# Kernel optimization log

Hardware: AMD Instinct MI355X
Metric: run time of the kernel (lower is better)

The kernel has to match this reference:

```python
import jax, jax.numpy as jnp
import numpy as np

N_NODES = 100000
N_EDGES = 1600000
NODE_DIM = 64
HIDDEN = 64
T = 11


def _init_linear(key, d_in, d_out, bias=True):
    kw, kb = jax.random.split(key)
    lim = 1.0 / np.sqrt(d_in)
    W = jax.random.uniform(kw, (d_in, d_out), jnp.float32, -lim, lim)
    if bias:
        b = jax.random.uniform(kb, (d_out,), jnp.float32, -lim, lim)
        return W, b
    return W


def setup_inputs() -> dict:
    key = jax.random.key(0)
    ks = jax.random.split(key, 10)
    x = jax.random.normal(ks[0], (N_NODES, NODE_DIM), jnp.float32)
    edge_index = jax.random.randint(ks[1], (2, N_EDGES), 0, N_NODES, jnp.int64)
    time_span = jnp.arange(T, dtype=jnp.float32)
    # SAGEConv params: W_neigh (lin_l, with bias) applied to mean-aggregated
    # neighbors, W_root (lin_r, no bias) applied to the node itself.
    W1n, b1 = _init_linear(ks[2], NODE_DIM, HIDDEN)
    W1r = _init_linear(ks[3], NODE_DIM, HIDDEN, bias=False)
    W2n, b2 = _init_linear(ks[4], HIDDEN, HIDDEN)
    W2r = _init_linear(ks[5], HIDDEN, HIDDEN, bias=False)
    W3n, b3 = _init_linear(ks[6], HIDDEN, NODE_DIM)
    W3r = _init_linear(ks[7], HIDDEN, NODE_DIM, bias=False)
    Wd, bd = _init_linear(ks[8], NODE_DIM, 2)
    return {
        "x": x, "edge_index": edge_index, "time_span": time_span,
        "W1n": W1n, "b1": b1, "W1r": W1r,
        "W2n": W2n, "b2": b2, "W2r": W2r,
        "W3n": W3n, "b3": b3, "W3r": W3r,
        "Wd": Wd, "bd": bd,
    }


def _sage_conv(x, src, dst, deg_inv, Wn, bn, Wr):
    # gather source features, mean-aggregate onto targets (PyG SAGEConv 'mean')
    agg = jax.ops.segment_sum(x[src], dst, num_segments=N_NODES)  # [N, d]
    mean = agg * deg_inv  # zero for isolated nodes
    return mean @ Wn + bn + x @ Wr


def reference(x, edge_index, time_span, W1n, b1, W1r, W2n, b2, W2r,
              W3n, b3, W3r, Wd, bd):
    src, dst = edge_index[0], edge_index[1]
    deg = jax.ops.segment_sum(jnp.ones((N_EDGES,), jnp.float32), dst,
                              num_segments=N_NODES)
    deg_inv = jnp.where(deg > 0, 1.0 / jnp.maximum(deg, 1.0), 0.0)[:, None]

    def ode_func(h):
        h1 = jax.nn.relu(_sage_conv(h, src, dst, deg_inv, W1n, b1, W1r))
        h2 = jax.nn.relu(_sage_conv(h1, src, dst, deg_inv, W2n, b2, W2r))
        return _sage_conv(h2, src, dst, deg_inv, W3n, b3, W3r)

    dts = time_span[1:] - time_span[:-1]  # euler fixed-step per interval

    def step(h, dt):
        h_new = h + dt * ode_func(h)
        return h_new, h_new

    _, xs = jax.lax.scan(step, x, dts)
    solution = jnp.concatenate([x[None], xs], axis=0)  # [T, N, node_dim]
    trajectories = solution @ Wd + bd  # [T, N, 2]
    return trajectories, solution
```

## Files before the change

kernel.cpp:

```cpp
#include <hip/hip_runtime.h>

#define NN 100000
#define NE 1600000
#define DIM 64
#define TT 11
#define NB_SCAN 391

typedef unsigned short u16;
typedef unsigned int u32;

__device__ __forceinline__ u32 pack_bf16(float a, float b) {
    u32 ua = __float_as_uint(a);
    ua += 0x7fff + ((ua >> 16) & 1);
    u32 ub = __float_as_uint(b);
    ub += 0x7fff + ((ub >> 16) & 1);
    return (ua >> 16) | (ub & 0xffff0000u);
}

__global__ void k_deg(const int* __restrict__ dst, int* __restrict__ deg) {
    int e = blockIdx.x * blockDim.x + threadIdx.x;
    if (e < NE) atomicAdd(&deg[dst[e]], 1);
}

__global__ __launch_bounds__(256) void k_bsum(const int* __restrict__ deg,
                                              int* __restrict__ bsum) {
    __shared__ int s[256];
    int t = threadIdx.x;
    int i = blockIdx.x * 256 + t;
    s[t] = (i < NN) ? deg[i] : 0;
    __syncthreads();
    for (int off = 128; off >= 1; off >>= 1) {
        if (t < off) s[t] += s[t + off];
        __syncthreads();
    }
    if (t == 0) bsum[blockIdx.x] = s[0];
}

__global__ __launch_bounds__(512) void k_scan1(const int* __restrict__ bsum,
                                               int* __restrict__ bpre) {
    __shared__ int s[512];
    int t = threadIdx.x;
    int v0 = (t < NB_SCAN) ? bsum[t] : 0;
    s[t] = v0;
    __syncthreads();
    for (int off = 1; off < 512; off <<= 1) {
        int v = (t >= off) ? s[t - off] : 0;
        __syncthreads();
        s[t] += v;
        __syncthreads();
    }
    if (t < NB_SCAN) bpre[t] = s[t] - v0;
}

__global__ __launch_bounds__(256) void k_rowptr(const int* __restrict__ deg,
        const int* __restrict__ bpre, int* __restrict__ row_ptr,
        int* __restrict__ cursor, float* __restrict__ deg_inv) {
    __shared__ int s[256];
    int t = threadIdx.x;
    int i = blockIdx.x * 256 + t;
    int d = (i < NN) ? deg[i] : 0;
    s[t] = d;
    __syncthreads();
    for (int off = 1; off < 256; off <<= 1) {
        int v = (t >= off) ? s[t - off] : 0;
        __syncthreads();
        s[t] += v;
        __syncthreads();
    }
    if (i < NN) {
        int excl = bpre[blockIdx.x] + s[t] - d;
        row_ptr[i] = excl;
        cursor[i] = excl;
        deg_inv[i] = d > 0 ? 1.0f / (float)d : 0.0f;
        if (i == NN - 1) row_ptr[NN] = excl + d;
    }
}

__global__ void k_fill(const int* __restrict__ src, const int* __restrict__ dst,
        int* __restrict__ cursor, int* __restrict__ csr_src) {
    int e = blockIdx.x * blockDim.x + threadIdx.x;
    if (e < NE) {
        int p = atomicAdd(&cursor[dst[e]], 1);
        csr_src[p] = src[e];
    }
}

__global__ __launch_bounds__(256) void k_gather(const u16* __restrict__ hb,
        const int* __restrict__ row_ptr, const int* __restrict__ csr_src,
        const float* __restrict__ deg_inv, float* __restrict__ M) {
    int wid = (int)((blockIdx.x * blockDim.x + threadIdx.x) >> 6);
    int lane = threadIdx.x & 63;
    if (wid >= NN) return;
    int sub = lane >> 3;
    int d4 = lane & 7;
    int b = row_ptr[wid], e = row_ptr[wid + 1];
    float di = deg_inv[wid];
    float a0[8] = {0, 0, 0, 0, 0, 0, 0, 0};
    float a1[8] = {0, 0, 0, 0, 0, 0, 0, 0};
    int i = b;
    for (; i + 16 <= e; i += 16) {
        int n0 = csr_src[i + sub];
        int n1 = csr_src[i + 8 + sub];
        uint4 v0 = *(const uint4*)(hb + ((size_t)n0 << 6) + d4 * 8);
        uint4 v1 = *(const uint4*)(hb + ((size_t)n1 << 6) + d4 * 8);
        const u32* w0 = (const u32*)&v0;
        const u32* w1 = (const u32*)&v1;
#pragma unroll
        for (int w = 0; w < 4; ++w) {
            a0[2 * w]     += __uint_as_float(w0[w] << 16);
            a0[2 * w + 1] += __uint_as_float(w0[w] & 0xffff0000u);
            a1[2 * w]     += __uint_as_float(w1[w] << 16);
            a1[2 * w + 1] += __uint_as_float(w1[w] & 0xffff0000u);
        }
    }
    if (i + 8 <= e) {
        int n0 = csr_src[i + sub];
        uint4 v0 = *(const uint4*)(hb + ((size_t)n0 << 6) + d4 * 8);
        const u32* w0 = (const u32*)&v0;
#pragma unroll
        for (int w = 0; w < 4; ++w) {
            a0[2 * w]     += __uint_as_float(w0[w] << 16);
            a0[2 * w + 1] += __uint_as_float(w0[w] & 0xffff0000u);
        }
        i += 8;
    }
    if (sub < e - i) {
        int n1 = csr_src[i + sub];
        uint4 v1 = *(const uint4*)(hb + ((size_t)n1 << 6) + d4 * 8);
        const u32* w1 = (const u32*)&v1;
#pragma unroll
        for (int w = 0; w < 4; ++w) {
            a1[2 * w]     += __uint_as_float(w1[w] << 16);
            a1[2 * w + 1] += __uint_as_float(w1[w] & 0xffff0000u);
        }
    }
    float s[8];
#pragma unroll
    for (int k = 0; k < 8; ++k) {
        float v = a0[k] + a1[k];
        v += __shfl_xor(v, 32);
        v += __shfl_xor(v, 16);
        v += __shfl_xor(v, 8);
        s[k] = v * di;
    }
    if (lane < 8) {
        float4* mr = (float4*)(M + ((size_t)wid << 6)) + d4 * 2;
        mr[0] = make_float4(s[0], s[1], s[2], s[3]);
        mr[1] = make_float4(s[4], s[5], s[6], s[7]);
    }
}

template <int MODE>
__global__ __launch_bounds__(256) void k_transform(
        const float* __restrict__ M, const float* __restrict__ H,
        const float* __restrict__ Wn, const float* __restrict__ bias,
        const float* __restrict__ Wr, const float* __restrict__ prev,
        const float* __restrict__ ts, int tstep, float* __restrict__ out,
        u16* __restrict__ out_b,
        const float* __restrict__ Wd, const float* __restrict__ bd,
        float* __restrict__ traj) {
    __shared__ float Ws[128 * 64];
    __shared__ float tp0[MODE ? 128 * 9 : 1];
    __shared__ float tp1[MODE ? 128 * 9 : 1];
    int tid = threadIdx.x;
    {
        const float4* wn4 = (const float4*)Wn;
        const float4* wr4 = (const float4*)Wr;
        float4* ws4 = (float4*)Ws;
        for (int i = tid; i < 2048; i += 256)
            ws4[i] = (i < 1024) ? wn4[i] : wr4[i - 1024];
    }
    __syncthreads();
    int jg = tid & 7, ng = tid >> 3;
    int nbase = blockIdx.x * 128 + ng * 4;
    int j0 = jg * 8;
    float acc[4][8];
#pragma unroll
    for (int i = 0; i < 4; ++i)
#pragma unroll
        for (int j = 0; j < 8; ++j) acc[i][j] = bias[j0 + j];
    int nidx[4];
    bool valid[4];
#pragma unroll
    for (int i = 0; i < 4; ++i) {
        int n = nbase + i;
        valid[i] = n < NN;
        nidx[i] = valid[i] ? n : 0;
    }
#pragma unroll 1
    for (int ph = 0; ph < 2; ++ph) {
        const float* A = ph ? H : M;
        int wofs = ph ? 64 * 64 : 0;
        for (int k0 = 0; k0 < 64; k0 += 4) {
            float a[4][4];
#pragma unroll
            for (int i = 0; i < 4; ++i)
                *(float4*)a[i] = *(const float4*)(A + (size_t)nidx[i] * 64 + k0);
#pragma unroll
            for (int kk = 0; kk < 4; ++kk) {
                float w[8];
                *(float4*)&w[0] = *(float4*)&Ws[wofs + (k0 + kk) * 64 + j0];
                *(float4*)&w[4] = *(float4*)&Ws[wofs + (k0 + kk) * 64 + j0 + 4];
#pragma unroll
                for (int i = 0; i < 4; ++i)
#pragma unroll
                    for (int j = 0; j < 8; ++j)
                        acc[i][j] = fmaf(a[i][kk], w[j], acc[i][j]);
            }
        }
    }
    float dt = 0.f, wd0[8], wd1[8];
    if (MODE == 1) {
        dt = ts[tstep + 1] - ts[tstep];
#pragma unroll
        for (int j = 0; j < 8; ++j) {
            wd0[j] = Wd[(j0 + j) * 2 + 0];
            wd1[j] = Wd[(j0 + j) * 2 + 1];
        }
    }
#pragma unroll
    for (int i = 0; i < 4; ++i) {
        float o[8];
        float p0 = 0.f, p1 = 0.f;
#pragma unroll
        for (int j = 0; j < 8; ++j) {
            float v = acc[i][j];
            if (MODE == 0) v = fmaxf(v, 0.f);
            else v = prev[(size_t)nidx[i] * 64 + j0 + j] + dt * v;
            o[j] = v;
            if (MODE == 1) { p0 = fmaf(v, wd0[j], p0); p1 = fmaf(v, wd1[j], p1); }
        }
        if (MODE == 1) {
            tp0[(ng * 4 + i) * 9 + jg] = p0;
            tp1[(ng * 4 + i) * 9 + jg] = p1;
        }
        if (valid[i]) {
            *(float4*)(out + (size_t)nidx[i] * 64 + j0) = *(float4*)&o[0];
            *(float4*)(out + (size_t)nidx[i] * 64 + j0 + 4) = *(float4*)&o[4];
            uint4 pb;
            pb.x = pack_bf16(o[0], o[1]);
            pb.y = pack_bf16(o[2], o[3]);
            pb.z = pack_bf16(o[4], o[5]);
            pb.w = pack_bf16(o[6], o[7]);
            *(uint4*)(out_b + (size_t)nidx[i] * 64 + j0) = pb;
        }
    }
    if (MODE == 1) {
        __syncthreads();
        int node = tid >> 1, comp = tid & 1;
        const float* tp = comp ? tp1 : tp0;
        float s = bd[comp];
#pragma unroll
        for (int g = 0; g < 8; ++g) s += tp[node * 9 + g];
        int gnode = blockIdx.x * 128 + node;
        if (gnode < NN)
            traj[((size_t)(tstep + 1) * NN + gnode) * 2 + comp] = s;
    }
}

__global__ __launch_bounds__(256) void k_init(const float* __restrict__ x,
        const float* __restrict__ Wd, const float* __restrict__ bd,
        float* __restrict__ sol0, u16* __restrict__ xb,
        float* __restrict__ traj) {
    int n = blockIdx.x * blockDim.x + threadIdx.x;
    if (n >= NN) return;
    const float4* xr = (const float4*)(x + ((size_t)n << 6));
    float4* sr = (float4*)(sol0 + ((size_t)n << 6));
    uint4* br = (uint4*)(xb + ((size_t)n << 6));
    float p0 = bd[0], p1 = bd[1];
#pragma unroll
    for (int k8 = 0; k8 < 8; ++k8) {
        float4 v0 = xr[k8 * 2];
        float4 v1 = xr[k8 * 2 + 1];
        sr[k8 * 2] = v0;
        sr[k8 * 2 + 1] = v1;
        uint4 pb;
        pb.x = pack_bf16(v0.x, v0.y);
        pb.y = pack_bf16(v0.z, v0.w);
        pb.z = pack_bf16(v1.x, v1.y);
        pb.w = pack_bf16(v1.z, v1.w);
        br[k8] = pb;
        int k = k8 * 8;
        p0 = fmaf(v0.x, Wd[(k + 0) * 2], p0); p1 = fmaf(v0.x, Wd[(k + 0) * 2 + 1], p1);
        p0 = fmaf(v0.y, Wd[(k + 1) * 2], p0); p1 = fmaf(v0.y, Wd[(k + 1) * 2 + 1], p1);
        p0 = fmaf(v0.z, Wd[(k + 2) * 2], p0); p1 = fmaf(v0.z, Wd[(k + 2) * 2 + 1], p1);
        p0 = fmaf(v0.w, Wd[(k + 3) * 2], p0); p1 = fmaf(v0.w, Wd[(k + 3) * 2 + 1], p1);
        p0 = fmaf(v1.x, Wd[(k + 4) * 2], p0); p1 = fmaf(v1.x, Wd[(k + 4) * 2 + 1], p1);
        p0 = fmaf(v1.y, Wd[(k + 5) * 2], p0); p1 = fmaf(v1.y, Wd[(k + 5) * 2 + 1], p1);
        p0 = fmaf(v1.z, Wd[(k + 6) * 2], p0); p1 = fmaf(v1.z, Wd[(k + 6) * 2 + 1], p1);
        p0 = fmaf(v1.w, Wd[(k + 7) * 2], p0); p1 = fmaf(v1.w, Wd[(k + 7) * 2 + 1], p1);
    }
    traj[(size_t)n * 2 + 0] = p0;
    traj[(size_t)n * 2 + 1] = p1;
}

extern "C" void kernel_launch(void* const* d_in, const int* in_sizes, int n_in,
                              void* d_out, int out_size, void* d_ws, size_t ws_size,
                              hipStream_t stream) {
    const float* x = (const float*)d_in[0];
    const int* ei = (const int*)d_in[1];
    const float* ts = (const float*)d_in[2];
    const float* W1n = (const float*)d_in[3];
    const float* b1 = (const float*)d_in[4];
    const float* W1r = (const float*)d_in[5];
    const float* W2n = (const float*)d_in[6];
    const float* b2 = (const float*)d_in[7];
    const float* W2r = (const float*)d_in[8];
    const float* W3n = (const float*)d_in[9];
    const float* b3 = (const float*)d_in[10];
    const float* W3r = (const float*)d_in[11];
    const float* Wd = (const float*)d_in[12];
    const float* bd = (const float*)d_in[13];
    const int* src = ei;
    const int* dst = ei + NE;

    char* w = (char*)d_ws;
    int* deg = (int*)w;          w += (size_t)NN * 4;
    int* row_ptr = (int*)w;      w += (size_t)(NN + 1) * 4;
    int* cursor = (int*)w;       w += (size_t)NN * 4;
    float* deg_inv = (float*)w;  w += (size_t)NN * 4;
    int* bsum = (int*)w;         w += (size_t)512 * 4;
    int* bpre = (int*)w;         w += (size_t)512 * 4;
    int* csr = (int*)w;          w += (size_t)NE * 4;
    float* M = (float*)w;        w += (size_t)NN * DIM * 4;
    float* h1 = (float*)w;       w += (size_t)NN * DIM * 4;
    float* h2 = (float*)w;       w += (size_t)NN * DIM * 4;
    u16* hb0 = (u16*)w;          w += (size_t)NN * DIM * 2;
    u16* hb1 = (u16*)w;          w += (size_t)NN * DIM * 2;
    u16* hb2 = (u16*)w;          w += (size_t)NN * DIM * 2;

    float* traj = (float*)d_out;
    float* sol = traj + (size_t)TT * NN * 2;

    hipMemsetAsync(deg, 0, (size_t)NN * 4, stream);
    k_deg<<<(NE + 255) / 256, 256, 0, stream>>>(dst, deg);
    k_bsum<<<NB_SCAN, 256, 0, stream>>>(deg, bsum);
    k_scan1<<<1, 512, 0, stream>>>(bsum, bpre);
    k_rowptr<<<NB_SCAN, 256, 0, stream>>>(deg, bpre, row_ptr, cursor, deg_inv);
    k_fill<<<(NE + 255) / 256, 256, 0, stream>>>(src, dst, cursor, csr);
    k_init<<<NB_SCAN, 256, 0, stream>>>(x, Wd, bd, sol, hb0, traj);

    const int GB = (NN * 64 + 255) / 256;
    const int TB = (NN + 127) / 128;
    for (int t = 0; t < TT - 1; ++t) {
        float* st = sol + (size_t)t * NN * DIM;
        float* sn = st + (size_t)NN * DIM;
        k_gather<<<GB, 256, 0, stream>>>(hb0, row_ptr, csr, deg_inv, M);
        k_transform<0><<<TB, 256, 0, stream>>>(M, st, W1n, b1, W1r, nullptr, ts, t, h1, hb1, Wd, bd, traj);
        k_gather<<<GB, 256, 0, stream>>>(hb1, row_ptr, csr, deg_inv, M);
        k_transform<0><<<TB, 256, 0, stream>>>(M, h1, W2n, b2, W2r, nullptr, ts, t, h2, hb2, Wd, bd, traj);
        k_gather<<<GB, 256, 0, stream>>>(hb2, row_ptr, csr, deg_inv, M);
        k_transform<1><<<TB, 256, 0, stream>>>(M, h2, W3n, b3, W3r, st, ts, t, sn, hb0, Wd, bd, traj);
    }
}
```

Before: 2.811 ms.

## Fuse neighbor gather into transform kernel via shared-memory bf16 aggregate tile

Merges the separate gather and transform kernels into one k_conv kernel: each block first aggregates neighbor means for its 128 nodes into a bf16 shared-memory tile, then runs the dense transform from shared memory. This removes the global M buffer round-trip (write then read of NN×64 floats) and halves kernel launches. The cost is lower gather parallelism (one block of 4 waves walks 128 nodes serially, 782 blocks total) and an extra bf16 rounding of the mean aggregate. The trajectory scratch is aliased onto the weight tile after a sync, and occupancy is pinned with a launch bound of 3 blocks per SIMD.

```diff
diff --git a/kernel.cpp b/kernel.cpp
--- a/kernel.cpp
+++ b/kernel.cpp
@@ -15,6 +15,9 @@
     u32 ub = __float_as_uint(b);
     ub += 0x7fff + ((ub >> 16) & 1);
     return (ua >> 16) | (ub & 0xffff0000u);
+}
+__device__ __forceinline__ float bf2f(u16 v) {
+    return __uint_as_float(((u32)v) << 16);
 }
 
 __global__ void k_deg(const int* __restrict__ dst, int* __restrict__ deg) {
@@ -85,83 +88,20 @@
     }
 }
 
-__global__ __launch_bounds__(256) void k_gather(const u16* __restrict__ hb,
+#define MS_LD 68
+template <int MODE>
+__global__ __launch_bounds__(256, 3) void k_conv(
+        const u16* __restrict__ hb, const float* __restrict__ H,
         const int* __restrict__ row_ptr, const int* __restrict__ csr_src,
-        const float* __restrict__ deg_inv, float* __restrict__ M) {
-    int wid = (int)((blockIdx.x * blockDim.x + threadIdx.x) >> 6);
-    int lane = threadIdx.x & 63;
-    if (wid >= NN) return;
-    int sub = lane >> 3;
-    int d4 = lane & 7;
-    int b = row_ptr[wid], e = row_ptr[wid + 1];
-    float di = deg_inv[wid];
-    float a0[8] = {0, 0, 0, 0, 0, 0, 0, 0};
-    float a1[8] = {0, 0, 0, 0, 0, 0, 0, 0};
-    int i = b;
-    for (; i + 16 <= e; i += 16) {
-        int n0 = csr_src[i + sub];
-        int n1 = csr_src[i + 8 + sub];
-        uint4 v0 = *(const uint4*)(hb + ((size_t)n0 << 6) + d4 * 8);
-        uint4 v1 = *(const uint4*)(hb + ((size_t)n1 << 6) + d4 * 8);
-        const u32* w0 = (const u32*)&v0;
-        const u32* w1 = (const u32*)&v1;
-#pragma unroll
-        for (int w = 0; w < 4; ++w) {
-            a0[2 * w]     += __uint_as_float(w0[w] << 16);
-            a0[2 * w + 1] += __uint_as_float(w0[w] & 0xffff0000u);
-            a1[2 * w]     += __uint_as_float(w1[w] << 16);
-            a1[2 * w + 1] += __uint_as_float(w1[w] & 0xffff0000u);
-        }
-    }
-    if (i + 8 <= e) {
-        int n0 = csr_src[i + sub];
-        uint4 v0 = *(const uint4*)(hb + ((size_t)n0 << 6) + d4 * 8);
-        const u32* w0 = (const u32*)&v0;
-#pragma unroll
-        for (int w = 0; w < 4; ++w) {
-            a0[2 * w]     += __uint_as_float(w0[w] << 16);
-            a0[2 * w + 1] += __uint_as_float(w0[w] & 0xffff0000u);
-        }
-        i += 8;
-    }
-    if (sub < e - i) {
-        int n1 = csr_src[i + sub];
-        uint4 v1 = *(const uint4*)(hb + ((size_t)n1 << 6) + d4 * 8);
-        const u32* w1 = (const u32*)&v1;
-#pragma unroll
-        for (int w = 0; w < 4; ++w) {
-            a1[2 * w]     += __uint_as_float(w1[w] << 16);
-            a1[2 * w + 1] += __uint_as_float(w1[w] & 0xffff0000u);
-        }
-    }
-    float s[8];
-#pragma unroll
-    for (int k = 0; k < 8; ++k) {
-        float v = a0[k] + a1[k];
-        v += __shfl_xor(v, 32);
-        v += __shfl_xor(v, 16);
-        v += __shfl_xor(v, 8);
-        s[k] = v * di;
-    }
-    if (lane < 8) {
-        float4* mr = (float4*)(M + ((size_t)wid << 6)) + d4 * 2;
-        mr[0] = make_float4(s[0], s[1], s[2], s[3]);
-        mr[1] = make_float4(s[4], s[5], s[6], s[7]);
-    }
-}
-
-template <int MODE>
-__global__ __launch_bounds__(256) void k_transform(
-        const float* __restrict__ M, const float* __restrict__ H,
+        const float* __restrict__ deg_inv,
         const float* __restrict__ Wn, const float* __restrict__ bias,
         const float* __restrict__ Wr, const float* __restrict__ prev,
-        const float* __restrict__ ts, int tstep, float* __restrict__ out,
-        u16* __restrict__ out_b,
+        const float* __restrict__ ts, int tstep,
+        float* __restrict__ out, u16* __restrict__ out_b,
         const float* __restrict__ Wd, const float* __restrict__ bd,
         float* __restrict__ traj) {
     __shared__ float Ws[128 * 64];
-    __shared__ float tp0[MODE ? 128 * 9 : 1];
-    __shared__ float tp1[MODE ? 128 * 9 : 1];
+    __shared__ u16 Ms[128 * MS_LD];
     int tid = threadIdx.x;
     {
         const float4* wn4 = (const float4*)Wn;
@@ -170,9 +110,77 @@
         for (int i = tid; i < 2048; i += 256)
             ws4[i] = (i < 1024) ? wn4[i] : wr4[i - 1024];
     }
+    int wv = tid >> 6, lane = tid & 63;
+    int sub = lane >> 3, d4 = lane & 7;
+    for (int ni = 0; ni < 32; ++ni) {
+        int lrow = wv * 32 + ni;
+        int node = blockIdx.x * 128 + lrow;
+        if (node >= NN) break;
+        int b = row_ptr[node], e = row_ptr[node + 1];
+        float di = deg_inv[node];
+        float a0[8] = {0, 0, 0, 0, 0, 0, 0, 0};
+        float a1[8] = {0, 0, 0, 0, 0, 0, 0, 0};
+        int i = b;
+        for (; i + 16 <= e; i += 16) {
+            int n0 = csr_src[i + sub];
+            int n1 = csr_src[i + 8 + sub];
+            uint4 v0 = *(const uint4*)(hb + ((size_t)n0 << 6) + d4 * 8);
+            uint4 v1 = *(const uint4*)(hb + ((size_t)n1 << 6) + d4 * 8);
+            const u32* w0 = (const u32*)&v0;
+            const u32* w1 = (const u32*)&v1;
+#pragma unroll
+            for (int w = 0; w < 4; ++w) {
+                a0[2 * w]     += __uint_as_float(w0[w] << 16);
+                a0[2 * w + 1] += __uint_as_float(w0[w] & 0xffff0000u);
+                a1[2 * w]     += __uint_as_float(w1[w] << 16);
+                a1[2 * w + 1] += __uint_as_float(w1[w] & 0xffff0000u);
+            }
+        }
+        if (i + 8 <= e) {
+            int n0 = csr_src[i + sub];
+            uint4 v0 = *(const uint4*)(hb + ((size_t)n0 << 6) + d4 * 8);
+            const u32* w0 = (const u32*)&v0;
+#pragma unroll
+            for (int w = 0; w < 4; ++w) {
+                a0[2 * w]     += __uint_as_float(w0[w] << 16);
+                a0[2 * w + 1] += __uint_as_float(w0[w] & 0xffff0000u);
+            }
+            i += 8;
+        }
+        if (sub < e - i) {
+            int n1 = csr_src[i + sub];
+            uint4 v1 = *(const uint4*)(hb + ((size_t)n1 << 6) + d4 * 8);
+            const u32* w1 = (const u32*)&v1;
+#pragma unroll
+            for (int w = 0; w < 4; ++w) {
+                a1[2 * w]     += __uint_as_float(w1[w] << 16);
+                a1[2 * w + 1] += __uint_as_float(w1[w] & 0xffff0000u);
+            }
+        }
+        float s[8];
+#pragma unroll
+        for (int k = 0; k < 8; ++k) {
+            float v = a0[k] + a1[k];
+            v += __shfl_xor(v, 32);
+            v += __shfl_xor(v, 16);
+            v += __shfl_xor(v, 8);
+            s[k] = v * di;
+        }
+        if (lane < 8) {
+            uint2 pa, pb;
+            pa.x = pack_bf16(s[0], s[1]);
+            pa.y = pack_bf16(s[2], s[3]);
+            pb.x = pack_bf16(s[4], s[5]);
+            pb.y = pack_bf16(s[6], s[7]);
+            u16* mp = &Ms[lrow * MS_LD + d4 * 8];
+            *(uint2*)mp = pa;
+            *(uint2*)(mp + 4) = pb;
+        }
+    }
     __syncthreads();
     int jg = tid & 7, ng = tid >> 3;
     int nbase = blockIdx.x * 128 + ng * 4;
+    int lbase = ng * 4;
     int j0 = jg * 8;
     float acc[4][8];
 #pragma unroll
@@ -187,26 +195,41 @@
         valid[i] = n < NN;
         nidx[i] = valid[i] ? n : 0;
     }
-#pragma unroll 1
-    for (int ph = 0; ph < 2; ++ph) {
-        const float* A = ph ? H : M;
-        int wofs = ph ? 64 * 64 : 0;
-        for (int k0 = 0; k0 < 64; k0 += 4) {
-            float a[4][4];
+    for (int k0 = 0; k0 < 64; k0 += 4) {
+        float a[4][4];
+#pragma unroll
+        for (int i = 0; i < 4; ++i) {
+            ushort4 r = *(const ushort4*)&Ms[(lbase + i) * MS_LD + k0];
+            a[i][0] = bf2f(r.x); a[i][1] = bf2f(r.y);
+            a[i][2] = bf2f(r.z); a[i][3] = bf2f(r.w);
+        }
+#pragma unroll
+        for (int kk = 0; kk < 4; ++kk) {
+            float w[8];
+            *(float4*)&w[0] = *(float4*)&Ws[(k0 + kk) * 64 + j0];
+            *(float4*)&w[4] = *(float4*)&Ws[(k0 + kk) * 64 + j0 + 4];
 #pragma unroll
             for (int i = 0; i < 4; ++i)
-                *(float4*)a[i] = *(const float4*)(A + (size_t)nidx[i] * 64 + k0);
-#pragma unroll
-            for (int kk = 0; kk < 4; ++kk) {
-                float w[8];
-                *(float4*)&w[0] = *(float4*)&Ws[wofs + (k0 + kk) * 64 + j0];
-                *(float4*)&w[4] = *(float4*)&Ws[wofs + (k0 + kk) * 64 + j0 + 4];
-#pragma unroll
-                for (int i = 0; i < 4; ++i)
-#pragma unroll
-                    for (int j = 0; j < 8; ++j)
-                        acc[i][j] = fmaf(a[i][kk], w[j], acc[i][j]);
-            }
+#pragma unroll
+                for (int j = 0; j < 8; ++j)
+                    acc[i][j] = fmaf(a[i][kk], w[j], acc[i][j]);
+        }
+    }
+    for (int k0 = 0; k0 < 64; k0 += 4) {
+        float a[4][4];
+#pragma unroll
+        for (int i = 0; i < 4; ++i)
+            *(float4*)a[i] = *(const float4*)(H + (size_t)nidx[i] * 64 + k0);
+#pragma unroll
+        for (int kk = 0; kk < 4; ++kk) {
+            float w[8];
+            *(float4*)&w[0] = *(float4*)&Ws[4096 + (k0 + kk) * 64 + j0];
+            *(float4*)&w[4] = *(float4*)&Ws[4096 + (k0 + kk) * 64 + j0 + 4];
+#pragma unroll
+            for (int i = 0; i < 4; ++i)
+#pragma unroll
+                for (int j = 0; j < 8; ++j)
+                    acc[i][j] = fmaf(a[i][kk], w[j], acc[i][j]);
         }
     }
     float dt = 0.f, wd0[8], wd1[8];
@@ -217,7 +240,10 @@
             wd0[j] = Wd[(j0 + j) * 2 + 0];
             wd1[j] = Wd[(j0 + j) * 2 + 1];
         }
-    }
+        __syncthreads();
+    }
+    float* tp0 = Ws;
+    float* tp1 = Ws + 128 * 9;
 #pragma unroll
     for (int i = 0; i < 4; ++i) {
         float o[8];
@@ -322,7 +348,6 @@
     int* bsum = (int*)w;         w += (size_t)512 * 4;
     int* bpre = (int*)w;         w += (size_t)512 * 4;
     int* csr = (int*)w;          w += (size_t)NE * 4;
-    float* M = (float*)w;        w += (size_t)NN * DIM * 4;
     float* h1 = (float*)w;       w += (size_t)NN * DIM * 4;
     float* h2 = (float*)w;       w += (size_t)NN * DIM * 4;
     u16* hb0 = (u16*)w;          w += (size_t)NN * DIM * 2;
@@ -340,16 +365,15 @@
     k_fill<<<(NE + 255) / 256, 256, 0, stream>>>(src, dst, cursor, csr);
     k_init<<<NB_SCAN, 256, 0, stream>>>(x, Wd, bd, sol, hb0, traj);
 
-    const int GB = (NN * 64 + 255) / 256;
     const int TB = (NN + 127) / 128;
     for (int t = 0; t < TT - 1; ++t) {
         float* st = sol + (size_t)t * NN * DIM;
         float* sn = st + (size_t)NN * DIM;
-        k_gather<<<GB, 256, 0, stream>>>(hb0, row_ptr, csr, deg_inv, M);
-        k_transform<0><<<TB, 256, 0, stream>>>(M, st, W1n, b1, W1r, nullptr, ts, t, h1, hb1, Wd, bd, traj);
-        k_gather<<<GB, 256, 0, stream>>>(hb1, row_ptr, csr, deg_inv, M);
-        k_transform<0><<<TB, 256, 0, stream>>>(M, h1, W2n, b2, W2r, nullptr, ts, t, h2, hb2, Wd, bd, traj);
-        k_gather<<<GB, 256, 0, stream>>>(hb2, row_ptr, csr, deg_inv, M);
-        k_transform<1><<<TB, 256, 0, stream>>>(M, h2, W3n, b3, W3r, st, ts, t, sn, hb0, Wd, bd, traj);
-    }
-}
+        k_conv<0><<<TB, 256, 0, stream>>>(hb0, st, row_ptr, csr, deg_inv,
+                W1n, b1, W1r, nullptr, ts, t, h1, hb1, Wd, bd, traj);
+        k_conv<0><<<TB, 256, 0, stream>>>(hb1, h1, row_ptr, csr, deg_inv,
+                W2n, b2, W2r, nullptr, ts, t, h2, hb2, Wd, bd, traj);
+        k_conv<1><<<TB, 256, 0, stream>>>(hb2, h2, row_ptr, csr, deg_inv,
+                W3n, b3, W3r, st, ts, t, sn, hb0, Wd, bd, traj);
+    }
+}
```

After: 4.693 ms. +66.9%, slower.

## Use bf16 activations in transform and bucket CSR neighbors by source chunk

Applied to the files above, without the earlier changes.

Stores the mean-aggregated features in bf16 and has the transform kernels read bf16 copies of both aggregated and root features. This halves their read traffic and drops the fp32 h1/h2 intermediate writes. The CSR build now orders each node's neighbor list by source-index chunk, so gathers touch nearby rows together and cache locality should improve. In exchange, the root term loses precision through bf16 rounding, and the setup needs a larger per-node chunk count array plus an extra memset and atomics.

```diff
diff --git a/kernel.cpp b/kernel.cpp
--- a/kernel.cpp
+++ b/kernel.cpp
@@ -5,6 +5,8 @@
 #define DIM 64
 #define TT 11
 #define NB_SCAN 391
+#define NCH 13
+#define CST 16
 
 typedef unsigned short u16;
 typedef unsigned int u32;
@@ -16,10 +18,18 @@
     ub += 0x7fff + ((ub >> 16) & 1);
     return (ua >> 16) | (ub & 0xffff0000u);
 }
-
-__global__ void k_deg(const int* __restrict__ dst, int* __restrict__ deg) {
+__device__ __forceinline__ float bf2f(u16 v) {
+    return __uint_as_float(((u32)v) << 16);
+}
+
+__global__ void k_degc(const int* __restrict__ src, const int* __restrict__ dst,
+                       int* __restrict__ deg, int* __restrict__ degc) {
     int e = blockIdx.x * blockDim.x + threadIdx.x;
-    if (e < NE) atomicAdd(&deg[dst[e]], 1);
+    if (e < NE) {
+        int d = dst[e], c = src[e] >> 13;
+        atomicAdd(&deg[d], 1);
+        atomicAdd(&degc[d * CST + c], 1);
+    }
 }
 
 __global__ __launch_bounds__(256) void k_bsum(const int* __restrict__ deg,
@@ -53,8 +63,9 @@
 }
 
 __global__ __launch_bounds__(256) void k_rowptr(const int* __restrict__ deg,
-        const int* __restrict__ bpre, int* __restrict__ row_ptr,
-        int* __restrict__ cursor, float* __restrict__ deg_inv) {
+        const int* __restrict__ degc, const int* __restrict__ bpre,
+        int* __restrict__ row_ptr, int* __restrict__ cursor16,
+        float* __restrict__ deg_inv) {
     __shared__ int s[256];
     int t = threadIdx.x;
     int i = blockIdx.x * 256 + t;
@@ -70,24 +81,30 @@
     if (i < NN) {
         int excl = bpre[blockIdx.x] + s[t] - d;
         row_ptr[i] = excl;
-        cursor[i] = excl;
         deg_inv[i] = d > 0 ? 1.0f / (float)d : 0.0f;
+        int run = excl;
+#pragma unroll
+        for (int c = 0; c < NCH; ++c) {
+            cursor16[i * CST + c] = run;
+            run += degc[i * CST + c];
+        }
         if (i == NN - 1) row_ptr[NN] = excl + d;
     }
 }
 
-__global__ void k_fill(const int* __restrict__ src, const int* __restrict__ dst,
-        int* __restrict__ cursor, int* __restrict__ csr_src) {
+__global__ void k_fillc(const int* __restrict__ src, const int* __restrict__ dst,
+        int* __restrict__ cursor16, int* __restrict__ csr_src) {
     int e = blockIdx.x * blockDim.x + threadIdx.x;
     if (e < NE) {
-        int p = atomicAdd(&cursor[dst[e]], 1);
-        csr_src[p] = src[e];
+        int sv = src[e];
+        int p = atomicAdd(&cursor16[dst[e] * CST + (sv >> 13)], 1);
+        csr_src[p] = sv;
     }
 }
 
 __global__ __launch_bounds__(256) void k_gather(const u16* __restrict__ hb,
         const int* __restrict__ row_ptr, const int* __restrict__ csr_src,
-        const float* __restrict__ deg_inv, float* __restrict__ M) {
+        const float* __restrict__ deg_inv, u16* __restrict__ Mb) {
     int wid = (int)((blockIdx.x * blockDim.x + threadIdx.x) >> 6);
     int lane = threadIdx.x & 63;
     if (wid >= NN) return;
@@ -144,15 +161,18 @@
         s[k] = v * di;
     }
     if (lane < 8) {
-        float4* mr = (float4*)(M + ((size_t)wid << 6)) + d4 * 2;
-        mr[0] = make_float4(s[0], s[1], s[2], s[3]);
-        mr[1] = make_float4(s[4], s[5], s[6], s[7]);
+        uint4 p;
+        p.x = pack_bf16(s[0], s[1]);
+        p.y = pack_bf16(s[2], s[3]);
+        p.z = pack_bf16(s[4], s[5]);
+        p.w = pack_bf16(s[6], s[7]);
+        *(uint4*)(Mb + ((size_t)wid << 6) + d4 * 8) = p;
     }
 }
 
 template <int MODE>
 __global__ __launch_bounds__(256) void k_transform(
-        const float* __restrict__ M, const float* __restrict__ H,
+        const u16* __restrict__ Mb, const u16* __restrict__ Hb,
         const float* __restrict__ Wn, const float* __restrict__ bias,
         const float* __restrict__ Wr, const float* __restrict__ prev,
         const float* __restrict__ ts, int tstep, float* __restrict__ out,
@@ -189,13 +209,16 @@
     }
 #pragma unroll 1
     for (int ph = 0; ph < 2; ++ph) {
-        const float* A = ph ? H : M;
+        const u16* A = ph ? Hb : Mb;
         int wofs = ph ? 64 * 64 : 0;
         for (int k0 = 0; k0 < 64; k0 += 4) {
             float a[4][4];
 #pragma unroll
-            for (int i = 0; i < 4; ++i)
-                *(float4*)a[i] = *(const float4*)(A + (size_t)nidx[i] * 64 + k0);
+            for (int i = 0; i < 4; ++i) {
+                ushort4 r = *(const ushort4*)(A + ((size_t)nidx[i] << 6) + k0);
+                a[i][0] = bf2f(r.x); a[i][1] = bf2f(r.y);
+                a[i][2] = bf2f(r.z); a[i][3] = bf2f(r.w);
+            }
 #pragma unroll
             for (int kk = 0; kk < 4; ++kk) {
                 float w[8];
@@ -235,8 +258,10 @@
             tp1[(ng * 4 + i) * 9 + jg] = p1;
         }
         if (valid[i]) {
-            *(float4*)(out + (size_t)nidx[i] * 64 + j0) = *(float4*)&o[0];
-            *(float4*)(out + (size_t)nidx[i] * 64 + j0 + 4) = *(float4*)&o[4];
+            if (MODE == 1) {
+                *(float4*)(out + (size_t)nidx[i] * 64 + j0) = *(float4*)&o[0];
+                *(float4*)(out + (size_t)nidx[i] * 64 + j0 + 4) = *(float4*)&o[4];
+            }
             uint4 pb;
             pb.x = pack_bf16(o[0], o[1]);
             pb.y = pack_bf16(o[2], o[3]);
@@ -316,15 +341,14 @@
 
     char* w = (char*)d_ws;
     int* deg = (int*)w;          w += (size_t)NN * 4;
+    int* degc = (int*)w;         w += (size_t)NN * CST * 4;
     int* row_ptr = (int*)w;      w += (size_t)(NN + 1) * 4;
-    int* cursor = (int*)w;       w += (size_t)NN * 4;
+    int* cursor16 = (int*)w;     w += (size_t)NN * CST * 4;
     float* deg_inv = (float*)w;  w += (size_t)NN * 4;
     int* bsum = (int*)w;         w += (size_t)512 * 4;
     int* bpre = (int*)w;         w += (size_t)512 * 4;
     int* csr = (int*)w;          w += (size_t)NE * 4;
-    float* M = (float*)w;        w += (size_t)NN * DIM * 4;
-    float* h1 = (float*)w;       w += (size_t)NN * DIM * 4;
-    float* h2 = (float*)w;       w += (size_t)NN * DIM * 4;
+    u16* Mb = (u16*)w;           w += (size_t)NN * DIM * 2;
     u16* hb0 = (u16*)w;          w += (size_t)NN * DIM * 2;
     u16* hb1 = (u16*)w;          w += (size_t)NN * DIM * 2;
     u16* hb2 = (u16*)w;          w += (size_t)NN * DIM * 2;
@@ -332,12 +356,12 @@
     float* traj = (float*)d_out;
     float* sol = traj + (size_t)TT * NN * 2;
 
-    hipMemsetAsync(deg, 0, (size_t)NN * 4, stream);
-    k_deg<<<(NE + 255) / 256, 256, 0, stream>>>(dst, deg);
+    hipMemsetAsync(deg, 0, (size_t)NN * (CST + 1) * 4, stream);
+    k_degc<<<(NE + 255) / 256, 256, 0, stream>>>(src, dst, deg, degc);
     k_bsum<<<NB_SCAN, 256, 0, stream>>>(deg, bsum);
     k_scan1<<<1, 512, 0, stream>>>(bsum, bpre);
-    k_rowptr<<<NB_SCAN, 256, 0, stream>>>(deg, bpre, row_ptr, cursor, deg_inv);
-    k_fill<<<(NE + 255) / 256, 256, 0, stream>>>(src, dst, cursor, csr);
+    k_rowptr<<<NB_SCAN, 256, 0, stream>>>(deg, degc, bpre, row_ptr, cursor16, deg_inv);
+    k_fillc<<<(NE + 255) / 256, 256, 0, stream>>>(src, dst, cursor16, csr);
     k_init<<<NB_SCAN, 256, 0, stream>>>(x, Wd, bd, sol, hb0, traj);
 
     const int GB = (NN * 64 + 255) / 256;
@@ -345,11 +369,14 @@
     for (int t = 0; t < TT - 1; ++t) {
         float* st = sol + (size_t)t * NN * DIM;
         float* sn = st + (size_t)NN * DIM;
-        k_gather<<<GB, 256, 0, stream>>>(hb0, row_ptr, csr, deg_inv, M);
-        k_transform<0><<<TB, 256, 0, stream>>>(M, st, W1n, b1, W1r, nullptr, ts, t, h1, hb1, Wd, bd, traj);
-        k_gather<<<GB, 256, 0, stream>>>(hb1, row_ptr, csr, deg_inv, M);
-        k_transform<0><<<TB, 256, 0, stream>>>(M, h1, W2n, b2, W2r, nullptr, ts, t, h2, hb2, Wd, bd, traj);
-        k_gather<<<GB, 256, 0, stream>>>(hb2, row_ptr, csr, deg_inv, M);
-        k_transform<1><<<TB, 256, 0, stream>>>(M, h2, W3n, b3, W3r, st, ts, t, sn, hb0, Wd, bd, traj);
-    }
-}
+        k_gather<<<GB, 256, 0, stream>>>(hb0, row_ptr, csr, deg_inv, Mb);
+        k_transform<0><<<TB, 256, 0, stream>>>(Mb, hb0, W1n, b1, W1r, nullptr,
+                ts, t, nullptr, hb1, Wd, bd, traj);
+        k_gather<<<GB, 256, 0, stream>>>(hb1, row_ptr, csr, deg_inv, Mb);
+        k_transform<0><<<TB, 256, 0, stream>>>(Mb, hb1, W2n, b2, W2r, nullptr,
+                ts, t, nullptr, hb2, Wd, bd, traj);
+        k_gather<<<GB, 256, 0, stream>>>(hb2, row_ptr, csr, deg_inv, Mb);
+        k_transform<1><<<TB, 256, 0, stream>>>(Mb, hb2, W3n, b3, W3r, st,
+                ts, t, sn, hb0, Wd, bd, traj);
+    }
+}
```

Result: faster. 2.725 ms (-3.1%).

## Use bf16 MFMA for SAGE transforms and keep intermediates in bf16

Applied to the files above, without the earlier changes.

Replaces the fp32 FMA-based dense transform with bf16 MFMA 16x16x32 instructions, using weights pre-transposed and packed to bf16 by a new prep kernel. The gather now writes the mean aggregate as bf16, and the transform reads bf16 node features directly, so the fp32 M, h1 and h2 buffers and their writes are dropped. The epilogue is staged through LDS so each thread handles half a node row, and the trajectory projection uses a shuffle reduction. The intent is to cut memory traffic and ALU time in the transform. The trade-off is bf16 rounding of the root-term inputs and of the aggregates, which lowers precision.

```diff
diff --git a/kernel.cpp b/kernel.cpp
--- a/kernel.cpp
+++ b/kernel.cpp
@@ -8,6 +8,8 @@
 
 typedef unsigned short u16;
 typedef unsigned int u32;
+typedef __attribute__((ext_vector_type(8))) short bf16x8;
+typedef __attribute__((ext_vector_type(4))) float f32x4;
 
 __device__ __forceinline__ u32 pack_bf16(float a, float b) {
     u32 ua = __float_as_uint(a);
@@ -85,9 +87,27 @@
     }
 }
 
+__global__ __launch_bounds__(256) void k_wprep(
+        const float* __restrict__ W1n, const float* __restrict__ W1r,
+        const float* __restrict__ W2n, const float* __restrict__ W2r,
+        const float* __restrict__ W3n, const float* __restrict__ W3r,
+        u16* __restrict__ Wt) {
+    const float* Ws[6] = {W1n, W1r, W2n, W2r, W3n, W3r};
+    const float* W = Ws[blockIdx.x];
+    u16* o = Wt + blockIdx.x * 4096;
+    int t = threadIdx.x;
+    int n = t >> 2, kg = (t & 3) * 16;
+    u32 pk[8];
+#pragma unroll
+    for (int j = 0; j < 8; ++j)
+        pk[j] = pack_bf16(W[(kg + 2 * j) * 64 + n], W[(kg + 2 * j + 1) * 64 + n]);
+    *(uint4*)(o + n * 64 + kg)     = make_uint4(pk[0], pk[1], pk[2], pk[3]);
+    *(uint4*)(o + n * 64 + kg + 8) = make_uint4(pk[4], pk[5], pk[6], pk[7]);
+}
+
 __global__ __launch_bounds__(256) void k_gather(const u16* __restrict__ hb,
         const int* __restrict__ row_ptr, const int* __restrict__ csr_src,
-        const float* __restrict__ deg_inv, float* __restrict__ M) {
+        const float* __restrict__ deg_inv, u16* __restrict__ Mb) {
     int wid = (int)((blockIdx.x * blockDim.x + threadIdx.x) >> 6);
     int lane = threadIdx.x & 63;
     if (wid >= NN) return;
@@ -144,117 +164,157 @@
         s[k] = v * di;
     }
     if (lane < 8) {
-        float4* mr = (float4*)(M + ((size_t)wid << 6)) + d4 * 2;
-        mr[0] = make_float4(s[0], s[1], s[2], s[3]);
-        mr[1] = make_float4(s[4], s[5], s[6], s[7]);
+        uint4 p;
+        p.x = pack_bf16(s[0], s[1]);
+        p.y = pack_bf16(s[2], s[3]);
+        p.z = pack_bf16(s[4], s[5]);
+        p.w = pack_bf16(s[6], s[7]);
+        *(uint4*)(Mb + ((size_t)wid << 6) + d4 * 8) = p;
     }
 }
 
 template <int MODE>
 __global__ __launch_bounds__(256) void k_transform(
-        const float* __restrict__ M, const float* __restrict__ H,
-        const float* __restrict__ Wn, const float* __restrict__ bias,
-        const float* __restrict__ Wr, const float* __restrict__ prev,
+        const u16* __restrict__ Mb, const u16* __restrict__ Hb,
+        const u16* __restrict__ Wtn, const float* __restrict__ bias,
+        const u16* __restrict__ Wtr, const float* __restrict__ prev,
         const float* __restrict__ ts, int tstep, float* __restrict__ out,
         u16* __restrict__ out_b,
         const float* __restrict__ Wd, const float* __restrict__ bd,
         float* __restrict__ traj) {
-    __shared__ float Ws[128 * 64];
-    __shared__ float tp0[MODE ? 128 * 9 : 1];
-    __shared__ float tp1[MODE ? 128 * 9 : 1];
+    __shared__ float Ls[4][32 * 68];
+    __shared__ float WdS[128];
     int tid = threadIdx.x;
+    if (MODE == 1 && tid < 128) WdS[tid] = Wd[tid];
+    int wv = tid >> 6, lane = tid & 63;
+    int r16 = lane & 15, kq = lane >> 4;
+    int nodeW = blockIdx.x * 128 + wv * 32;
+    size_t rowA[2];
+#pragma unroll
+    for (int rt = 0; rt < 2; ++rt) {
+        int n = nodeW + rt * 16 + r16;
+        rowA[rt] = (size_t)(n < NN ? n : NN - 1) << 6;
+    }
+    f32x4 acc[2][4];
+#pragma unroll
+    for (int ct = 0; ct < 4; ++ct) {
+        float bc = bias[ct * 16 + r16];
+#pragma unroll
+        for (int rt = 0; rt < 2; ++rt)
+            acc[rt][ct] = (f32x4){bc, bc, bc, bc};
+    }
     {
-        const float4* wn4 = (const float4*)Wn;
-        const float4* wr4 = (const float4*)Wr;
-        float4* ws4 = (float4*)Ws;
-        for (int i = tid; i < 2048; i += 256)
-            ws4[i] = (i < 1024) ? wn4[i] : wr4[i - 1024];
-    }
+        bf16x8 a[2][2], b[4][2];
+#pragma unroll
+        for (int rt = 0; rt < 2; ++rt)
+#pragma unroll
+            for (int kh = 0; kh < 2; ++kh)
+                a[rt][kh] = *(const bf16x8*)(Mb + rowA[rt] + kh * 32 + kq * 8);
+#pragma unroll
+        for (int ct = 0; ct < 4; ++ct)
+#pragma unroll
+            for (int kh = 0; kh < 2; ++kh)
+                b[ct][kh] = *(const bf16x8*)(Wtn + (ct * 16 + r16) * 64 + kh * 32 + kq * 8);
+#pragma unroll
+        for (int rt = 0; rt < 2; ++rt)
+#pragma unroll
+            for (int ct = 0; ct < 4; ++ct)
+#pragma unroll
+                for (int kh = 0; kh < 2; ++kh)
+                    acc[rt][ct] = __builtin_amdgcn_mfma_f32_16x16x32_bf16(
+                        a[rt][kh], b[ct][kh], acc[rt][ct], 0, 0, 0);
+    }
+    {
+        bf16x8 a[2][2], b[4][2];
+#pragma unroll
+        for (int rt = 0; rt < 2; ++rt)
+#pragma unroll
+            for (int kh = 0; kh < 2; ++kh)
+                a[rt][kh] = *(const bf16x8*)(Hb + rowA[rt] + kh * 32 + kq * 8);
+#pragma unroll
+        for (int ct = 0; ct < 4; ++ct)
+#pragma unroll
+            for (int kh = 0; kh < 2; ++kh)
+                b[ct][kh] = *(const bf16x8*)(Wtr + (ct * 16 + r16) * 64 + kh * 32 + kq * 8);
+#pragma unroll
+        for (int rt = 0; rt < 2; ++rt)
+#pragma unroll
+            for (int ct = 0; ct < 4; ++ct)
+#pragma unroll
+                for (int kh = 0; kh < 2; ++kh)
+                    acc[rt][ct] = __builtin_amdgcn_mfma_f32_16x16x32_bf16(
+                        a[rt][kh], b[ct][kh], acc[rt][ct], 0, 0, 0);
+    }
+    float* L = Ls[wv];
+#pragma unroll
+    for (int rt = 0; rt < 2; ++rt)
+#pragma unroll
+        for (int ct = 0; ct < 4; ++ct)
+#pragma unroll
+            for (int j = 0; j < 4; ++j)
+                L[(rt * 16 + kq * 4 + j) * 68 + ct * 16 + r16] = acc[rt][ct][j];
     __syncthreads();
-    int jg = tid & 7, ng = tid >> 3;
-    int nbase = blockIdx.x * 128 + ng * 4;
-    int j0 = jg * 8;
-    float acc[4][8];
-#pragma unroll
-    for (int i = 0; i < 4; ++i)
-#pragma unroll
-        for (int j = 0; j < 8; ++j) acc[i][j] = bias[j0 + j];
-    int nidx[4];
-    bool valid[4];
-#pragma unroll
-    for (int i = 0; i < 4; ++i) {
-        int n = nbase + i;
-        valid[i] = n < NN;
-        nidx[i] = valid[i] ? n : 0;
-    }
-#pragma unroll 1
-    for (int ph = 0; ph < 2; ++ph) {
-        const float* A = ph ? H : M;
-        int wofs = ph ? 64 * 64 : 0;
-        for (int k0 = 0; k0 < 64; k0 += 4) {
-            float a[4][4];
-#pragma unroll
-            for (int i = 0; i < 4; ++i)
-                *(float4*)a[i] = *(const float4*)(A + (size_t)nidx[i] * 64 + k0);
-#pragma unroll
-            for (int kk = 0; kk < 4; ++kk) {
-                float w[8];
-                *(float4*)&w[0] = *(float4*)&Ws[wofs + (k0 + kk) * 64 + j0];
-                *(float4*)&w[4] = *(float4*)&Ws[wofs + (k0 + kk) * 64 + j0 + 4];
-#pragma unroll
-                for (int i = 0; i < 4; ++i)
-#pragma unroll
-                    for (int j = 0; j < 8; ++j)
-                        acc[i][j] = fmaf(a[i][kk], w[j], acc[i][j]);
-            }
-        }
-    }
-    float dt = 0.f, wd0[8], wd1[8];
+    int nl = tid >> 1, hf = tid & 1;
+    int gnode = blockIdx.x * 128 + nl;
+    const float* Lrow = &Ls[nl >> 5][(nl & 31) * 68 + hf * 32];
+    float dt = 0.f;
+    if (MODE == 1) dt = ts[tstep + 1] - ts[tstep];
+    float v[32];
+    float p0 = 0.f, p1 = 0.f;
+    bool ok = gnode < NN;
+    size_t gofs = ((size_t)(ok ? gnode : 0) << 6) + hf * 32;
+#pragma unroll
+    for (int i = 0; i < 32; ++i) {
+        float x = Lrow[i];
+        if (MODE == 0) x = fmaxf(x, 0.f);
+        v[i] = x;
+    }
     if (MODE == 1) {
-        dt = ts[tstep + 1] - ts[tstep];
-#pragma unroll
-        for (int j = 0; j < 8; ++j) {
-            wd0[j] = Wd[(j0 + j) * 2 + 0];
-            wd1[j] = Wd[(j0 + j) * 2 + 1];
-        }
-    }
-#pragma unroll
-    for (int i = 0; i < 4; ++i) {
-        float o[8];
-        float p0 = 0.f, p1 = 0.f;
-#pragma unroll
-        for (int j = 0; j < 8; ++j) {
-            float v = acc[i][j];
-            if (MODE == 0) v = fmaxf(v, 0.f);
-            else v = prev[(size_t)nidx[i] * 64 + j0 + j] + dt * v;
-            o[j] = v;
-            if (MODE == 1) { p0 = fmaf(v, wd0[j], p0); p1 = fmaf(v, wd1[j], p1); }
-        }
+#pragma unroll
+        for (int i4 = 0; i4 < 8; ++i4) {
+            float4 pv = *(const float4*)(prev + gofs + i4 * 4);
+            v[i4 * 4 + 0] = pv.x + dt * v[i4 * 4 + 0];
+            v[i4 * 4 + 1] = pv.y + dt * v[i4 * 4 + 1];
+            v[i4 * 4 + 2] = pv.z + dt * v[i4 * 4 + 2];
+            v[i4 * 4 + 3] = pv.w + dt * v[i4 * 4 + 3];
+        }
+#pragma unroll
+        for (int i = 0; i < 32; ++i) {
+            p0 = fmaf(v[i], WdS[(hf * 32 + i) * 2 + 0], p0);
+            p1 = fmaf(v[i], WdS[(hf * 32 + i) * 2 + 1], p1);
+        }
+    }
+    if (ok) {
         if (MODE == 1) {
-            tp0[(ng * 4 + i) * 9 + jg] = p0;
-            tp1[(ng * 4 + i) * 9 + jg] = p1;
-        }
-        if (valid[i]) {
-            *(float4*)(out + (size_t)nidx[i] * 64 + j0) = *(float4*)&o[0];
-            *(float4*)(out + (size_t)nidx[i] * 64 + j0 + 4) = *(float4*)&o[4];
+#pragma unroll
+            for (int i4 = 0; i4 < 8; ++i4)
+                *(float4*)(out + gofs + i4 * 4) =
+                    make_float4(v[i4 * 4], v[i4 * 4 + 1], v[i4 * 4 + 2], v[i4 * 4 + 3]);
+        }
+#pragma unroll
+        for (int q = 0; q < 2; ++q) {
             uint4 pb;
-            pb.x = pack_bf16(o[0], o[1]);
-            pb.y = pack_bf16(o[2], o[3]);
-            pb.z = pack_bf16(o[4], o[5]);
-            pb.w = pack_bf16(o[6], o[7]);
-            *(uint4*)(out_b + (size_t)nidx[i] * 64 + j0) = pb;
+            pb.x = pack_bf16(v[q * 16 + 0], v[q * 16 + 1]);
+            pb.y = pack_bf16(v[q * 16 + 2], v[q * 16 + 3]);
+            pb.z = pack_bf16(v[q * 16 + 4], v[q * 16 + 5]);
+            pb.w = pack_bf16(v[q * 16 + 6], v[q * 16 + 7]);
+            uint4 pc;
+            pc.x = pack_bf16(v[q * 16 + 8], v[q * 16 + 9]);
+            pc.y = pack_bf16(v[q * 16 + 10], v[q * 16 + 11]);
+            pc.z = pack_bf16(v[q * 16 + 12], v[q * 16 + 13]);
+            pc.w = pack_bf16(v[q * 16 + 14], v[q * 16 + 15]);
+            *(uint4*)(out_b + gofs + q * 16)     = pb;
+            *(uint4*)(out_b + gofs + q * 16 + 8) = pc;
         }
     }
     if (MODE == 1) {
-        __syncthreads();
-        int node = tid >> 1, comp = tid & 1;
-        const float* tp = comp ? tp1 : tp0;
-        float s = bd[comp];
-#pragma unroll
-        for (int g = 0; g < 8; ++g) s += tp[node * 9 + g];
-        int gnode = blockIdx.x * 128 + node;
-        if (gnode < NN)
-            traj[((size_t)(tstep + 1) * NN + gnode) * 2 + comp] = s;
+        p0 += __shfl_xor(p0, 1);
+        p1 += __shfl_xor(p1, 1);
+        if (ok) {
+            size_t ti = ((size_t)(tstep + 1) * NN + gnode) * 2;
+            if (hf == 0) traj[ti + 0] = p0 + bd[0];
+            else         traj[ti + 1] = p1 + bd[1];
+        }
     }
 }
 
@@ -322,9 +382,8 @@
     int* bsum = (int*)w;         w += (size_t)512 * 4;
     int* bpre = (int*)w;         w += (size_t)512 * 4;
     int* csr = (int*)w;          w += (size_t)NE * 4;
-    float* M = (float*)w;        w += (size_t)NN * DIM * 4;
-    float* h1 = (float*)w;       w += (size_t)NN * DIM * 4;
-    float* h2 = (float*)w;       w += (size_t)NN * DIM * 4;
+    u16* Wt = (u16*)w;           w += (size_t)6 * 4096 * 2;
+    u16* Mb = (u16*)w;           w += (size_t)NN * DIM * 2;
     u16* hb0 = (u16*)w;          w += (size_t)NN * DIM * 2;
     u16* hb1 = (u16*)w;          w += (size_t)NN * DIM * 2;
     u16* hb2 = (u16*)w;          w += (size_t)NN * DIM * 2;
@@ -338,18 +397,29 @@
     k_scan1<<<1, 512, 0, stream>>>(bsum, bpre);
     k_rowptr<<<NB_SCAN, 256, 0, stream>>>(deg, bpre, row_ptr, cursor, deg_inv);
     k_fill<<<(NE + 255) / 256, 256, 0, stream>>>(src, dst, cursor, csr);
+    k_wprep<<<6, 256, 0, stream>>>(W1n, W1r, W2n, W2r, W3n, W3r, Wt);
     k_init<<<NB_SCAN, 256, 0, stream>>>(x, Wd, bd, sol, hb0, traj);
+
+    const u16* Wt1n = Wt;
+    const u16* Wt1r = Wt + 4096;
+    const u16* Wt2n = Wt + 2 * 4096;
+    const u16* Wt2r = Wt + 3 * 4096;
+    const u16* Wt3n = Wt + 4 * 4096;
+    const u16* Wt3r = Wt + 5 * 4096;
 
     const int GB = (NN * 64 + 255) / 256;
     const int TB = (NN + 127) / 128;
     for (int t = 0; t < TT - 1; ++t) {
         float* st = sol + (size_t)t * NN * DIM;
         float* sn = st + (size_t)NN * DIM;
-        k_gather<<<GB, 256, 0, stream>>>(hb0, row_ptr, csr, deg_inv, M);
-        k_transform<0><<<TB, 256, 0, stream>>>(M, st, W1n, b1, W1r, nullptr, ts, t, h1, hb1, Wd, bd, traj);
-        k_gather<<<GB, 256, 0, stream>>>(hb1, row_ptr, csr, deg_inv, M);
-        k_transform<0><<<TB, 256, 0, stream>>>(M, h1, W2n, b2, W2r, nullptr, ts, t, h2, hb2, Wd, bd, traj);
-        k_gather<<<GB, 256, 0, stream>>>(hb2, row_ptr, csr, deg_inv, M);
-        k_transform<1><<<TB, 256, 0, stream>>>(M, h2, W3n, b3, W3r, st, ts, t, sn, hb0, Wd, bd, traj);
-    }
-}
+        k_gather<<<GB, 256, 0, stream>>>(hb0, row_ptr, csr, deg_inv, Mb);
+        k_transform<0><<<TB, 256, 0, stream>>>(Mb, hb0, Wt1n, b1, Wt1r, nullptr,
+                ts, t, nullptr, hb1, Wd, bd, traj);
+        k_gather<<<GB, 256, 0, stream>>>(hb1, row_ptr, csr, deg_inv, Mb);
+        k_transform<0><<<TB, 256, 0, stream>>>(Mb, hb1, Wt2n, b2, Wt2r, nullptr,
+                ts, t, nullptr, hb2, Wd, bd, traj);
+        k_gather<<<GB, 256, 0, stream>>>(hb2, row_ptr, csr, deg_inv, Mb);
+        k_transform<1><<<TB, 256, 0, stream>>>(Mb, hb2, Wt3n, b3, Wt3r, st,
+                ts, t, sn, hb0, Wd, bd, traj);
+    }
+}
```

Result: faster. 2.287 ms, median of 2 (-18.7%).
